# Kernel optimization log

Hardware: AMD Instinct MI355X
Metric: run time of the kernel (lower is better)

## Reference

```python
import jax, jax.numpy as jnp
import numpy as np

E = 1024       # embedding_dim
HQ = 16        # num_q_heads
G = 4          # group_size
HK = HQ // G   # num_kv_heads = 4
D = E // HQ    # q_head_dim = 64
B, N = 2, 2048


def setup_inputs() -> dict:
    key = jax.random.key(0)
    kx, kq, kk, kv, ko = jax.random.split(key, 5)
    scale = 0.02
    return {
        "x": jax.random.normal(kx, (B, N, E), dtype=jnp.float32),
        # weights stored as (in, out); torch Linear computes x @ W.T, equivalent math
        "Wq": jax.random.normal(kq, (E, E), dtype=jnp.float32) * scale,
        "Wk": jax.random.normal(kk, (E, E // G), dtype=jnp.float32) * scale,
        "Wv": jax.random.normal(kv, (E, E // G), dtype=jnp.float32) * scale,
        "Wo": jax.random.normal(ko, (E, E), dtype=jnp.float32) * scale,
    }


def reference(x, Wq, Wk, Wv, Wo):
    b, n, _ = x.shape
    q = x @ Wq                      # (b, n, E)
    k = x @ Wk                      # (b, n, HK*D)
    v = x @ Wv                      # (b, n, HK*D)
    # 'b n (h d) -> b h n d' then 'b (h g) n d -> b g h n d'  (h outer, g inner)
    q = q.reshape(b, n, HQ, D).transpose(0, 2, 1, 3)          # (b, HQ, n, D)
    q = q.reshape(b, HK, G, n, D).transpose(0, 2, 1, 3, 4)    # (b, G, HK, n, D)
    k = k.reshape(b, n, HK, D).transpose(0, 2, 1, 3)          # (b, HK, n, D)
    v = v.reshape(b, n, HK, D).transpose(0, 2, 1, 3)          # (b, HK, n, D)

    scores = jnp.einsum('bghnd,bhsd->bghns', q, k) / jnp.sqrt(jnp.float32(D))
    causal = jnp.triu(jnp.ones((n, n), dtype=bool), k=1)      # True above diagonal
    scores = jnp.where(causal[None, None, None], -jnp.inf, scores)
    probs = jax.nn.softmax(scores, axis=-1)                   # dropout p=0 -> no-op
    out = jnp.einsum('bghns,bhsd->bghnd', probs, v)           # (b, G, HK, n, D)
    # 'b g h n d -> b n (h g) d -> b n (h g d)'
    out = out.transpose(0, 3, 2, 1, 4).reshape(b, n, E)
    return out @ Wo
```

## Files before the change

kernel.cpp:

```cpp
#include <hip/hip_runtime.h>
#include <hip/hip_bf16.h>
#include <math.h>

#define Bsz 2
#define Nseq 2048
#define Edim 1024
#define HQ 16
#define HK 4
#define Dh 64
#define ROWS (Bsz * Nseq)
#define QKVW 1536
#define SCL 0.1803368801111244f

typedef __attribute__((ext_vector_type(8))) short short8;
typedef __attribute__((ext_vector_type(4))) float f32x4;

union S8U { short8 s8; unsigned u[4]; };

__device__ __forceinline__ ushort f2bf_u(float f) {
    union { __hip_bfloat16 h; ushort u; } c;
    c.h = __float2bfloat16(f);
    return c.u;
}
__device__ __forceinline__ unsigned bfpk(float lo, float hi) {
    return ((unsigned)f2bf_u(hi) << 16) | (unsigned)f2bf_u(lo);
}

__device__ __forceinline__ void gld16(const void* g, void* l) {
    __builtin_amdgcn_global_load_lds(
        (const __attribute__((address_space(1))) unsigned*)g,
        (__attribute__((address_space(3))) unsigned*)l, 16, 0, 0);
}

__global__ __launch_bounds__(256) void castx(const float* __restrict__ x,
                                             ushort* __restrict__ xb) {
    size_t i = ((size_t)blockIdx.x * 256 + threadIdx.x) * 8;
    float4 a = *(const float4*)(x + i);
    float4 c = *(const float4*)(x + i + 4);
    short8 v;
    v[0] = f2bf_u(a.x); v[1] = f2bf_u(a.y); v[2] = f2bf_u(a.z); v[3] = f2bf_u(a.w);
    v[4] = f2bf_u(c.x); v[5] = f2bf_u(c.y); v[6] = f2bf_u(c.z); v[7] = f2bf_u(c.w);
    *(short8*)(xb + i) = v;
}

__global__ __launch_bounds__(256) void tcastAll(const float* __restrict__ Wq,
                                                const float* __restrict__ Wk,
                                                const float* __restrict__ Wv,
                                                const float* __restrict__ Wo,
                                                ushort* __restrict__ WqkvT,
                                                ushort* __restrict__ WoT) {
    __shared__ float tle[32][33];
    int bid = blockIdx.x;
    const float* src; ushort* dst; int N; float sc = 1.0f;
    if (bid < 1024)      { src = Wq; dst = WqkvT;                          N = 1024; sc = SCL; }
    else if (bid < 1280) { src = Wk; dst = WqkvT + (size_t)1024 * 1024;    N = 256;  bid -= 1024; }
    else if (bid < 1536) { src = Wv; dst = WqkvT + (size_t)1280 * 1024;    N = 256;  bid -= 1280; }
    else                 { src = Wo; dst = WoT;                            N = 1024; bid -= 1536; }
    int nj = N >> 5;
    int j0 = (bid % nj) * 32, k0 = (bid / nj) * 32;
    int tx = threadIdx.x & 31, ty = threadIdx.x >> 5;
#pragma unroll
    for (int i = ty; i < 32; i += 8)
        tle[i][tx] = src[(size_t)(k0 + i) * N + j0 + tx];
    __syncthreads();
#pragma unroll
    for (int i = ty; i < 32; i += 8)
        dst[(size_t)(j0 + i) * 1024 + k0 + tx] = f2bf_u(tle[tx][i] * sc);
}

template<int WRITE_BF16>
__global__ __launch_bounds__(256) void gemm_bt(const ushort* __restrict__ A,
                                               const ushort* __restrict__ BT,
                                               void* __restrict__ Cout,
                                               int M, int N, int K) {
    __shared__ __attribute__((aligned(16))) ushort As[2][4][128][8];
    __shared__ __attribute__((aligned(16))) ushort Bs[2][4][64][8];
    const int tid = threadIdx.x;
    const int l = tid & 63, li = l & 15, lg = l >> 4;
    const int w = tid >> 6;
    const int wr = w >> 1, wc = w & 1;
    const int row0 = blockIdx.y * 128, col0 = blockIdx.x * 64;

    f32x4 acc[4][2];
#pragma unroll
    for (int i = 0; i < 4; ++i)
#pragma unroll
        for (int j = 0; j < 2; ++j) {
            acc[i][j][0] = 0.f; acc[i][j][1] = 0.f;
            acc[i][j][2] = 0.f; acc[i][j][3] = 0.f;
        }

    const int nk = K >> 5;

#define G_STAGE(buf, kk)                                                        \
    {                                                                           \
        int k0 = (kk) << 5;                                                     \
        _Pragma("unroll")                                                       \
        for (int i = 0; i < 3; ++i) {                                           \
            int id = w + i * 4;                                                 \
            if (id < 8) {                                                       \
                int g = id >> 1, h = id & 1;                                    \
                gld16(A + (size_t)(row0 + h * 64 + l) * K + k0 + g * 8,         \
                      &As[buf][g][h * 64][0]);                                  \
            } else {                                                            \
                int g = id - 8;                                                 \
                gld16(BT + (size_t)(col0 + l) * K + k0 + g * 8,                 \
                      &Bs[buf][g][0][0]);                                       \
            }                                                                   \
        }                                                                       \
    }

    G_STAGE(0, 0);
    __syncthreads();
    int buf = 0;
    for (int kk = 0; kk < nk; ++kk) {
        if (kk + 1 < nk) G_STAGE(buf ^ 1, kk + 1);
        short8 af[4], bfr[2];
#pragma unroll
        for (int mt = 0; mt < 4; ++mt)
            af[mt] = *(const short8*)&As[buf][lg][wr * 64 + mt * 16 + li][0];
#pragma unroll
        for (int nt = 0; nt < 2; ++nt)
            bfr[nt] = *(const short8*)&Bs[buf][lg][wc * 32 + nt * 16 + li][0];
#pragma unroll
        for (int mt = 0; mt < 4; ++mt)
#pragma unroll
            for (int nt = 0; nt < 2; ++nt)
                acc[mt][nt] = __builtin_amdgcn_mfma_f32_16x16x32_bf16(
                    af[mt], bfr[nt], acc[mt][nt], 0, 0, 0);
        __syncthreads();
        buf ^= 1;
    }
#undef G_STAGE

    if (WRITE_BF16) {
        ushort* C = (ushort*)Cout;
#pragma unroll
        for (int mt = 0; mt < 4; ++mt)
#pragma unroll
            for (int r = 0; r < 4; ++r) {
                int rg = row0 + wr * 64 + mt * 16 + lg * 4 + r;
#pragma unroll
                for (int nt = 0; nt < 2; ++nt)
                    C[(size_t)rg * N + col0 + wc * 32 + nt * 16 + li] =
                        f2bf_u(acc[mt][nt][r]);
            }
    } else {
        float* C = (float*)Cout;
#pragma unroll
        for (int mt = 0; mt < 4; ++mt)
#pragma unroll
            for (int r = 0; r < 4; ++r) {
                int rg = row0 + wr * 64 + mt * 16 + lg * 4 + r;
#pragma unroll
                for (int nt = 0; nt < 2; ++nt)
                    C[(size_t)rg * N + col0 + wc * 32 + nt * 16 + li] =
                        acc[mt][nt][r];
            }
    }
}

__global__ __launch_bounds__(256) void attn_mfma(const ushort* __restrict__ qkv,
                                                 ushort* __restrict__ o) {
    __shared__ __attribute__((aligned(16))) char smem[40960];
    ushort (*Ks)[8][64][8] = (ushort (*)[8][64][8])smem;
    unsigned (*VtD)[2048]  = (unsigned (*)[2048])(smem + 16384);
    ushort (*Ps)[8][16][8] = (ushort (*)[8][16][8])(smem + 32768);

    const int tid = threadIdx.x;
    const int l = tid & 63, li = l & 15, lg = l >> 4;
    const int w = tid >> 6;
    const int bx = blockIdx.x;
    const int hq = blockIdx.y, b = blockIdx.z, hk = hq >> 2;

    const int kp = 2 * (tid & 31), d0v = (tid >> 5) * 8;
    const int gv = kp >> 3, prv = (kp & 7) >> 1;

    const ushort* base  = qkv + (size_t)b * Nseq * QKVW;
    const ushort* vbase = base + 1280 + hk * 64 + d0v;
    const int qloc = w * 16 + li;

    for (int hseg = 0; hseg < 2; ++hseg) {
        const int qt = hseg ? (31 - bx) : bx;
        const int r0 = qt * 64;

        short8 q8[2];
#pragma unroll
        for (int c = 0; c < 2; ++c)
            q8[c] = *(const short8*)(base + (size_t)(r0 + qloc) * QKVW +
                                     hq * 64 + (c * 4 + lg) * 8);

#pragma unroll
        for (int i = 0; i < 2; ++i) {
            int g = w + i * 4;
            gld16(base + (size_t)l * QKVW + 1024 + hk * 64 + g * 8,
                  &Ks[0][g][0][0]);
        }
        short8 va = *(const short8*)(vbase + (size_t)kp * QKVW);
        short8 vb = *(const short8*)(vbase + (size_t)(kp + 1) * QKVW);
        __syncthreads();
        {
            S8U ua, ub; ua.s8 = va; ub.s8 = vb;
#pragma unroll
            for (int j = 0; j < 4; ++j) {
                VtD[0][gv * 256 + (((d0v + 2 * j) * 4 + prv) ^ (gv << 2))] =
                    __builtin_amdgcn_perm(ub.u[j], ua.u[j], 0x05040100u);
                VtD[0][gv * 256 + (((d0v + 2 * j + 1) * 4 + prv) ^ (gv << 2))] =
                    __builtin_amdgcn_perm(ub.u[j], ua.u[j], 0x07060302u);
            }
        }
        __syncthreads();

        f32x4 oacc[4];
#pragma unroll
        for (int dt = 0; dt < 4; ++dt) {
            oacc[dt][0] = 0.f; oacc[dt][1] = 0.f;
            oacc[dt][2] = 0.f; oacc[dt][3] = 0.f;
        }
        float m = -INFINITY, lsum = 0.f;

        for (int t = 0; t <= qt; ++t) {
            const int cur = t & 1, nxt = cur ^ 1;
            const bool pre = (t < qt);
            short8 vna, vnb;
            if (pre) {
                const int s1 = (t + 1) * 64;
#pragma unroll
                for (int i = 0; i < 2; ++i) {
                    int g = w + i * 4;
                    gld16(base + (size_t)(s1 + l) * QKVW + 1024 + hk * 64 + g * 8,
                          &Ks[nxt][g][0][0]);
                }
                const ushort* vr = vbase + (size_t)(s1 + kp) * QKVW;
                vna = *(const short8*)vr;
                vnb = *(const short8*)(vr + QKVW);
            }

            f32x4 s[4];
#pragma unroll
            for (int kb = 0; kb < 4; ++kb) {
                s[kb][0] = 0.f; s[kb][1] = 0.f; s[kb][2] = 0.f; s[kb][3] = 0.f;
            }
#pragma unroll
            for (int c = 0; c < 2; ++c)
#pragma unroll
                for (int kb = 0; kb < 4; ++kb) {
                    short8 bk = *(const short8*)&Ks[cur][c * 4 + lg][kb * 16 + li][0];
                    s[kb] = __builtin_amdgcn_mfma_f32_16x16x32_bf16(bk, q8[c], s[kb], 0, 0, 0);
                }

            float p[16];
            const bool last = (t == qt);
#pragma unroll
            for (int kb = 0; kb < 4; ++kb)
#pragma unroll
                for (int r = 0; r < 4; ++r) {
                    float sv = s[kb][r];
                    if (last && (kb * 16 + lg * 4 + r > qloc)) sv = -INFINITY;
                    p[kb * 4 + r] = sv;
                }

            float mx = fmaxf(fmaxf(
                fmaxf(fmaxf(p[0], p[1]), fmaxf(p[2], p[3])),
                fmaxf(fmaxf(p[4], p[5]), fmaxf(p[6], p[7]))),
                fmaxf(fmaxf(fmaxf(p[8], p[9]), fmaxf(p[10], p[11])),
                      fmaxf(fmaxf(p[12], p[13]), fmaxf(p[14], p[15]))));
            mx = fmaxf(mx, __shfl_xor(mx, 16, 64));
            mx = fmaxf(mx, __shfl_xor(mx, 32, 64));

            if (__any(mx - m > 8.0f)) {
                float mn = fmaxf(m, mx);
                float al = exp2f(m - mn);
                m = mn;
                lsum *= al;
                float alr[4];
#pragma unroll
                for (int r = 0; r < 4; ++r) alr[r] = __shfl(al, lg * 4 + r, 64);
#pragma unroll
                for (int dt = 0; dt < 4; ++dt)
#pragma unroll
                    for (int r = 0; r < 4; ++r) oacc[dt][r] *= alr[r];
            }

            float sum = 0.f;
#pragma unroll
            for (int i = 0; i < 16; ++i) {
                float e = exp2f(p[i] - m);
                p[i] = e;
                sum += e;
            }
            sum += __shfl_xor(sum, 16, 64);
            sum += __shfl_xor(sum, 32, 64);
            lsum += sum;

#pragma unroll
            for (int kb = 0; kb < 4; ++kb) {
                unsigned lo = bfpk(p[kb * 4 + 0], p[kb * 4 + 1]);
                unsigned hi = bfpk(p[kb * 4 + 2], p[kb * 4 + 3]);
                *(unsigned long long*)&Ps[w][2 * kb + (lg >> 1)][li][(lg & 1) * 4] =
                    ((unsigned long long)hi << 32) | (unsigned long long)lo;
            }

            if (pre) {
                S8U ua, ub; ua.s8 = vna; ub.s8 = vnb;
#pragma unroll
                for (int j = 0; j < 4; ++j) {
                    VtD[nxt][gv * 256 + (((d0v + 2 * j) * 4 + prv) ^ (gv << 2))] =
                        __builtin_amdgcn_perm(ub.u[j], ua.u[j], 0x05040100u);
                    VtD[nxt][gv * 256 + (((d0v + 2 * j + 1) * 4 + prv) ^ (gv << 2))] =
                        __builtin_amdgcn_perm(ub.u[j], ua.u[j], 0x07060302u);
                }
            }

#pragma unroll
            for (int c = 0; c < 2; ++c) {
                short8 pa = *(const short8*)&Ps[w][c * 4 + lg][li][0];
#pragma unroll
                for (int dt = 0; dt < 4; ++dt) {
                    int g = c * 4 + lg, d = dt * 16 + li;
                    short8 bv = *(const short8*)(&VtD[cur][g * 256 + ((d * 4) ^ (g << 2))]);
                    oacc[dt] = __builtin_amdgcn_mfma_f32_16x16x32_bf16(pa, bv, oacc[dt], 0, 0, 0);
                }
            }
            __syncthreads();
        }

        float linv[4];
#pragma unroll
        for (int r = 0; r < 4; ++r) linv[r] = 1.0f / __shfl(lsum, lg * 4 + r, 64);
#pragma unroll
        for (int r = 0; r < 4; ++r) {
            int rg = b * Nseq + r0 + w * 16 + lg * 4 + r;
#pragma unroll
            for (int dt = 0; dt < 4; ++dt)
                o[(size_t)rg * Edim + hq * 64 + dt * 16 + li] =
                    f2bf_u(oacc[dt][r] * linv[r]);
        }
    }
}

extern "C" void kernel_launch(void* const* d_in, const int* in_sizes, int n_in,
                              void* d_out, int out_size, void* d_ws, size_t ws_size,
                              hipStream_t stream) {
    const float* x  = (const float*)d_in[0];
    const float* Wq = (const float*)d_in[1];
    const float* Wk = (const float*)d_in[2];
    const float* Wv = (const float*)d_in[3];
    const float* Wo = (const float*)d_in[4];

    ushort* ws    = (ushort*)d_ws;
    ushort* xb    = ws;
    ushort* WqkvT = xb + (size_t)ROWS * Edim;
    ushort* WoT   = WqkvT + (size_t)QKVW * Edim;
    ushort* qkv   = WoT + (size_t)Edim * Edim;
    ushort* at    = qkv + (size_t)ROWS * QKVW;

    castx<<<ROWS * Edim / (256 * 8), 256, 0, stream>>>(x, xb);
    tcastAll<<<2560, 256, 0, stream>>>(Wq, Wk, Wv, Wo, WqkvT, WoT);

    gemm_bt<1><<<dim3(QKVW / 64, ROWS / 128), 256, 0, stream>>>(
        xb, WqkvT, qkv, ROWS, QKVW, Edim);

    attn_mfma<<<dim3(Nseq / 128, HQ, Bsz), 256, 0, stream>>>(qkv, at);

    gemm_bt<0><<<dim3(Edim / 64, ROWS / 128), 256, 0, stream>>>(
        at, WoT, d_out, ROWS, Edim, Edim);
}
```

Before: 209.3 us.

## Merge prep kernels, deepen GEMM K-tile, process KV tiles in pairs in attention

Fuses the x cast and weight transpose-cast into one prep launch, saving a kernel launch. The GEMM now stages 64-wide K slices instead of 32, halving the barrier count per block. The attention kernel loads two 64-key tiles per iteration and does one online-softmax rescale per 128 keys, cutting syncs and rescale work. In exchange, shared memory grows to 72KB in attention, which may lower occupancy, and odd tile counts waste one fully masked 64-key tile.

```diff
diff --git a/kernel.cpp b/kernel.cpp
--- a/kernel.cpp
+++ b/kernel.cpp
@@ -32,25 +32,26 @@
         (__attribute__((address_space(3))) unsigned*)l, 16, 0, 0);
 }
 
-__global__ __launch_bounds__(256) void castx(const float* __restrict__ x,
-                                             ushort* __restrict__ xb) {
-    size_t i = ((size_t)blockIdx.x * 256 + threadIdx.x) * 8;
-    float4 a = *(const float4*)(x + i);
-    float4 c = *(const float4*)(x + i + 4);
-    short8 v;
-    v[0] = f2bf_u(a.x); v[1] = f2bf_u(a.y); v[2] = f2bf_u(a.z); v[3] = f2bf_u(a.w);
-    v[4] = f2bf_u(c.x); v[5] = f2bf_u(c.y); v[6] = f2bf_u(c.z); v[7] = f2bf_u(c.w);
-    *(short8*)(xb + i) = v;
-}
-
-__global__ __launch_bounds__(256) void tcastAll(const float* __restrict__ Wq,
-                                                const float* __restrict__ Wk,
-                                                const float* __restrict__ Wv,
-                                                const float* __restrict__ Wo,
-                                                ushort* __restrict__ WqkvT,
-                                                ushort* __restrict__ WoT) {
+__global__ __launch_bounds__(256) void prep(const float* __restrict__ x,
+                                            const float* __restrict__ Wq,
+                                            const float* __restrict__ Wk,
+                                            const float* __restrict__ Wv,
+                                            const float* __restrict__ Wo,
+                                            ushort* __restrict__ xb,
+                                            ushort* __restrict__ WqkvT,
+                                            ushort* __restrict__ WoT) {
+    if (blockIdx.x < 2048) {
+        size_t i = ((size_t)blockIdx.x * 256 + threadIdx.x) * 8;
+        float4 a = *(const float4*)(x + i);
+        float4 c = *(const float4*)(x + i + 4);
+        short8 v;
+        v[0] = f2bf_u(a.x); v[1] = f2bf_u(a.y); v[2] = f2bf_u(a.z); v[3] = f2bf_u(a.w);
+        v[4] = f2bf_u(c.x); v[5] = f2bf_u(c.y); v[6] = f2bf_u(c.z); v[7] = f2bf_u(c.w);
+        *(short8*)(xb + i) = v;
+        return;
+    }
     __shared__ float tle[32][33];
-    int bid = blockIdx.x;
+    int bid = blockIdx.x - 2048;
     const float* src; ushort* dst; int N; float sc = 1.0f;
     if (bid < 1024)      { src = Wq; dst = WqkvT;                          N = 1024; sc = SCL; }
     else if (bid < 1280) { src = Wk; dst = WqkvT + (size_t)1024 * 1024;    N = 256;  bid -= 1024; }
@@ -73,8 +74,8 @@
                                                const ushort* __restrict__ BT,
                                                void* __restrict__ Cout,
                                                int M, int N, int K) {
-    __shared__ __attribute__((aligned(16))) ushort As[2][4][128][8];
-    __shared__ __attribute__((aligned(16))) ushort Bs[2][4][64][8];
+    __shared__ __attribute__((aligned(16))) ushort As[2][8][128][8];
+    __shared__ __attribute__((aligned(16))) ushort Bs[2][8][64][8];
     const int tid = threadIdx.x;
     const int l = tid & 63, li = l & 15, lg = l >> 4;
     const int w = tid >> 6;
@@ -90,20 +91,20 @@
             acc[i][j][2] = 0.f; acc[i][j][3] = 0.f;
         }
 
-    const int nk = K >> 5;
+    const int nk = K >> 6;
 
 #define G_STAGE(buf, kk)                                                        \
     {                                                                           \
-        int k0 = (kk) << 5;                                                     \
+        int k0 = (kk) << 6;                                                     \
         _Pragma("unroll")                                                       \
-        for (int i = 0; i < 3; ++i) {                                           \
+        for (int i = 0; i < 6; ++i) {                                           \
             int id = w + i * 4;                                                 \
-            if (id < 8) {                                                       \
+            if (id < 16) {                                                      \
                 int g = id >> 1, h = id & 1;                                    \
                 gld16(A + (size_t)(row0 + h * 64 + l) * K + k0 + g * 8,         \
                       &As[buf][g][h * 64][0]);                                  \
             } else {                                                            \
-                int g = id - 8;                                                 \
+                int g = id - 16;                                                \
                 gld16(BT + (size_t)(col0 + l) * K + k0 + g * 8,                 \
                       &Bs[buf][g][0][0]);                                       \
             }                                                                   \
@@ -115,19 +116,22 @@
     int buf = 0;
     for (int kk = 0; kk < nk; ++kk) {
         if (kk + 1 < nk) G_STAGE(buf ^ 1, kk + 1);
-        short8 af[4], bfr[2];
-#pragma unroll
-        for (int mt = 0; mt < 4; ++mt)
-            af[mt] = *(const short8*)&As[buf][lg][wr * 64 + mt * 16 + li][0];
-#pragma unroll
-        for (int nt = 0; nt < 2; ++nt)
-            bfr[nt] = *(const short8*)&Bs[buf][lg][wc * 32 + nt * 16 + li][0];
-#pragma unroll
-        for (int mt = 0; mt < 4; ++mt)
+#pragma unroll
+        for (int ks = 0; ks < 2; ++ks) {
+            short8 af[4], bfr[2];
+#pragma unroll
+            for (int mt = 0; mt < 4; ++mt)
+                af[mt] = *(const short8*)&As[buf][ks * 4 + lg][wr * 64 + mt * 16 + li][0];
 #pragma unroll
             for (int nt = 0; nt < 2; ++nt)
-                acc[mt][nt] = __builtin_amdgcn_mfma_f32_16x16x32_bf16(
-                    af[mt], bfr[nt], acc[mt][nt], 0, 0, 0);
+                bfr[nt] = *(const short8*)&Bs[buf][ks * 4 + lg][wc * 32 + nt * 16 + li][0];
+#pragma unroll
+            for (int mt = 0; mt < 4; ++mt)
+#pragma unroll
+                for (int nt = 0; nt < 2; ++nt)
+                    acc[mt][nt] = __builtin_amdgcn_mfma_f32_16x16x32_bf16(
+                        af[mt], bfr[nt], acc[mt][nt], 0, 0, 0);
+        }
         __syncthreads();
         buf ^= 1;
     }
@@ -162,10 +166,10 @@
 
 __global__ __launch_bounds__(256) void attn_mfma(const ushort* __restrict__ qkv,
                                                  ushort* __restrict__ o) {
-    __shared__ __attribute__((aligned(16))) char smem[40960];
-    ushort (*Ks)[8][64][8] = (ushort (*)[8][64][8])smem;
-    unsigned (*VtD)[2048]  = (unsigned (*)[2048])(smem + 16384);
-    ushort (*Ps)[8][16][8] = (ushort (*)[8][16][8])(smem + 32768);
+    __shared__ __attribute__((aligned(16))) char smem[73728];
+    ushort (*Ks)[2][8][64][8] = (ushort (*)[2][8][64][8])smem;
+    unsigned (*VtD)[2][2048]  = (unsigned (*)[2][2048])(smem + 32768);
+    ushort (*Ps)[8][16][8]    = (ushort (*)[8][16][8])(smem + 65536);
 
     const int tid = threadIdx.x;
     const int l = tid & 63, li = l & 15, lg = l >> 4;
@@ -183,6 +187,7 @@
     for (int hseg = 0; hseg < 2; ++hseg) {
         const int qt = hseg ? (31 - bx) : bx;
         const int r0 = qt * 64;
+        const int npair = (qt + 2) >> 1;
 
         short8 q8[2];
 #pragma unroll
@@ -191,22 +196,29 @@
                                      hq * 64 + (c * 4 + lg) * 8);
 
 #pragma unroll
-        for (int i = 0; i < 2; ++i) {
-            int g = w + i * 4;
-            gld16(base + (size_t)l * QKVW + 1024 + hk * 64 + g * 8,
-                  &Ks[0][g][0][0]);
-        }
-        short8 va = *(const short8*)(vbase + (size_t)kp * QKVW);
-        short8 vb = *(const short8*)(vbase + (size_t)(kp + 1) * QKVW);
+        for (int i = 0; i < 4; ++i) {
+            int id = w + i * 4, tile = id >> 3, g = id & 7;
+            gld16(base + (size_t)(tile * 64 + l) * QKVW + 1024 + hk * 64 + g * 8,
+                  &Ks[0][tile][g][0][0]);
+        }
+        short8 v0a = *(const short8*)(vbase + (size_t)kp * QKVW);
+        short8 v0b = *(const short8*)(vbase + (size_t)(kp + 1) * QKVW);
+        short8 v1a = *(const short8*)(vbase + (size_t)(64 + kp) * QKVW);
+        short8 v1b = *(const short8*)(vbase + (size_t)(64 + kp + 1) * QKVW);
         __syncthreads();
         {
-            S8U ua, ub; ua.s8 = va; ub.s8 = vb;
+            S8U ua0, ub0, ua1, ub1;
+            ua0.s8 = v0a; ub0.s8 = v0b; ua1.s8 = v1a; ub1.s8 = v1b;
 #pragma unroll
             for (int j = 0; j < 4; ++j) {
-                VtD[0][gv * 256 + (((d0v + 2 * j) * 4 + prv) ^ (gv << 2))] =
-                    __builtin_amdgcn_perm(ub.u[j], ua.u[j], 0x05040100u);
-                VtD[0][gv * 256 + (((d0v + 2 * j + 1) * 4 + prv) ^ (gv << 2))] =
-                    __builtin_amdgcn_perm(ub.u[j], ua.u[j], 0x07060302u);
+                VtD[0][0][gv * 256 + (((d0v + 2 * j) * 4 + prv) ^ (gv << 2))] =
+                    __builtin_amdgcn_perm(ub0.u[j], ua0.u[j], 0x05040100u);
+                VtD[0][0][gv * 256 + (((d0v + 2 * j + 1) * 4 + prv) ^ (gv << 2))] =
+                    __builtin_amdgcn_perm(ub0.u[j], ua0.u[j], 0x07060302u);
+                VtD[0][1][gv * 256 + (((d0v + 2 * j) * 4 + prv) ^ (gv << 2))] =
+                    __builtin_amdgcn_perm(ub1.u[j], ua1.u[j], 0x05040100u);
+                VtD[0][1][gv * 256 + (((d0v + 2 * j + 1) * 4 + prv) ^ (gv << 2))] =
+                    __builtin_amdgcn_perm(ub1.u[j], ua1.u[j], 0x07060302u);
             }
         }
         __syncthreads();
@@ -219,52 +231,55 @@
         }
         float m = -INFINITY, lsum = 0.f;
 
-        for (int t = 0; t <= qt; ++t) {
-            const int cur = t & 1, nxt = cur ^ 1;
-            const bool pre = (t < qt);
-            short8 vna, vnb;
+        for (int pt = 0; pt < npair; ++pt) {
+            const int cur = pt & 1, nxt = cur ^ 1;
+            const bool pre = (pt + 1 < npair);
+            short8 vn0a, vn0b, vn1a, vn1b;
             if (pre) {
-                const int s1 = (t + 1) * 64;
-#pragma unroll
-                for (int i = 0; i < 2; ++i) {
-                    int g = w + i * 4;
-                    gld16(base + (size_t)(s1 + l) * QKVW + 1024 + hk * 64 + g * 8,
-                          &Ks[nxt][g][0][0]);
-                }
-                const ushort* vr = vbase + (size_t)(s1 + kp) * QKVW;
-                vna = *(const short8*)vr;
-                vnb = *(const short8*)(vr + QKVW);
-            }
-
-            f32x4 s[4];
-#pragma unroll
-            for (int kb = 0; kb < 4; ++kb) {
-                s[kb][0] = 0.f; s[kb][1] = 0.f; s[kb][2] = 0.f; s[kb][3] = 0.f;
-            }
-#pragma unroll
-            for (int c = 0; c < 2; ++c)
+                const int s1 = (pt + 1) * 128;
+#pragma unroll
+                for (int i = 0; i < 4; ++i) {
+                    int id = w + i * 4, tile = id >> 3, g = id & 7;
+                    gld16(base + (size_t)(s1 + tile * 64 + l) * QKVW + 1024 + hk * 64 + g * 8,
+                          &Ks[nxt][tile][g][0][0]);
+                }
+                vn0a = *(const short8*)(vbase + (size_t)(s1 + kp) * QKVW);
+                vn0b = *(const short8*)(vbase + (size_t)(s1 + kp + 1) * QKVW);
+                vn1a = *(const short8*)(vbase + (size_t)(s1 + 64 + kp) * QKVW);
+                vn1b = *(const short8*)(vbase + (size_t)(s1 + 64 + kp + 1) * QKVW);
+            }
+
+            float p[32];
+#pragma unroll
+            for (int tt = 0; tt < 2; ++tt) {
+                f32x4 s[4];
 #pragma unroll
                 for (int kb = 0; kb < 4; ++kb) {
-                    short8 bk = *(const short8*)&Ks[cur][c * 4 + lg][kb * 16 + li][0];
-                    s[kb] = __builtin_amdgcn_mfma_f32_16x16x32_bf16(bk, q8[c], s[kb], 0, 0, 0);
-                }
-
-            float p[16];
-            const bool last = (t == qt);
-#pragma unroll
-            for (int kb = 0; kb < 4; ++kb)
-#pragma unroll
-                for (int r = 0; r < 4; ++r) {
-                    float sv = s[kb][r];
-                    if (last && (kb * 16 + lg * 4 + r > qloc)) sv = -INFINITY;
-                    p[kb * 4 + r] = sv;
-                }
-
-            float mx = fmaxf(fmaxf(
-                fmaxf(fmaxf(p[0], p[1]), fmaxf(p[2], p[3])),
-                fmaxf(fmaxf(p[4], p[5]), fmaxf(p[6], p[7]))),
-                fmaxf(fmaxf(fmaxf(p[8], p[9]), fmaxf(p[10], p[11])),
-                      fmaxf(fmaxf(p[12], p[13]), fmaxf(p[14], p[15]))));
+                    s[kb][0] = 0.f; s[kb][1] = 0.f; s[kb][2] = 0.f; s[kb][3] = 0.f;
+                }
+#pragma unroll
+                for (int c = 0; c < 2; ++c)
+#pragma unroll
+                    for (int kb = 0; kb < 4; ++kb) {
+                        short8 bk = *(const short8*)&Ks[cur][tt][c * 4 + lg][kb * 16 + li][0];
+                        s[kb] = __builtin_amdgcn_mfma_f32_16x16x32_bf16(bk, q8[c], s[kb], 0, 0, 0);
+                    }
+                const int tglob = pt * 2 + tt;
+                const bool diag = (tglob == qt), over = (tglob > qt);
+#pragma unroll
+                for (int kb = 0; kb < 4; ++kb)
+#pragma unroll
+                    for (int r = 0; r < 4; ++r) {
+                        float sv = s[kb][r];
+                        if (over || (diag && (kb * 16 + lg * 4 + r > qloc)))
+                            sv = -INFINITY;
+                        p[tt * 16 + kb * 4 + r] = sv;
+                    }
+            }
+
+            float mx = p[0];
+#pragma unroll
+            for (int i = 1; i < 32; ++i) mx = fmaxf(mx, p[i]);
             mx = fmaxf(mx, __shfl_xor(mx, 16, 64));
             mx = fmaxf(mx, __shfl_xor(mx, 32, 64));
 
@@ -284,7 +299,7 @@
 
             float sum = 0.f;
 #pragma unroll
-            for (int i = 0; i < 16; ++i) {
+            for (int i = 0; i < 32; ++i) {
                 float e = exp2f(p[i] - m);
                 p[i] = e;
                 sum += e;
@@ -293,33 +308,40 @@
             sum += __shfl_xor(sum, 32, 64);
             lsum += sum;
 
-#pragma unroll
-            for (int kb = 0; kb < 4; ++kb) {
-                unsigned lo = bfpk(p[kb * 4 + 0], p[kb * 4 + 1]);
-                unsigned hi = bfpk(p[kb * 4 + 2], p[kb * 4 + 3]);
-                *(unsigned long long*)&Ps[w][2 * kb + (lg >> 1)][li][(lg & 1) * 4] =
-                    ((unsigned long long)hi << 32) | (unsigned long long)lo;
-            }
-
             if (pre) {
-                S8U ua, ub; ua.s8 = vna; ub.s8 = vnb;
+                S8U ua0, ub0, ua1, ub1;
+                ua0.s8 = vn0a; ub0.s8 = vn0b; ua1.s8 = vn1a; ub1.s8 = vn1b;
 #pragma unroll
                 for (int j = 0; j < 4; ++j) {
-                    VtD[nxt][gv * 256 + (((d0v + 2 * j) * 4 + prv) ^ (gv << 2))] =
-                        __builtin_amdgcn_perm(ub.u[j], ua.u[j], 0x05040100u);
-                    VtD[nxt][gv * 256 + (((d0v + 2 * j + 1) * 4 + prv) ^ (gv << 2))] =
-                        __builtin_amdgcn_perm(ub.u[j], ua.u[j], 0x07060302u);
-                }
-            }
-
-#pragma unroll
-            for (int c = 0; c < 2; ++c) {
-                short8 pa = *(const short8*)&Ps[w][c * 4 + lg][li][0];
-#pragma unroll
-                for (int dt = 0; dt < 4; ++dt) {
-                    int g = c * 4 + lg, d = dt * 16 + li;
-                    short8 bv = *(const short8*)(&VtD[cur][g * 256 + ((d * 4) ^ (g << 2))]);
-                    oacc[dt] = __builtin_amdgcn_mfma_f32_16x16x32_bf16(pa, bv, oacc[dt], 0, 0, 0);
+                    VtD[nxt][0][gv * 256 + (((d0v + 2 * j) * 4 + prv) ^ (gv << 2))] =
+                        __builtin_amdgcn_perm(ub0.u[j], ua0.u[j], 0x05040100u);
+                    VtD[nxt][0][gv * 256 + (((d0v + 2 * j + 1) * 4 + prv) ^ (gv << 2))] =
+                        __builtin_amdgcn_perm(ub0.u[j], ua0.u[j], 0x07060302u);
+                    VtD[nxt][1][gv * 256 + (((d0v + 2 * j) * 4 + prv) ^ (gv << 2))] =
+                        __builtin_amdgcn_perm(ub1.u[j], ua1.u[j], 0x05040100u);
+                    VtD[nxt][1][gv * 256 + (((d0v + 2 * j + 1) * 4 + prv) ^ (gv << 2))] =
+                        __builtin_amdgcn_perm(ub1.u[j], ua1.u[j], 0x07060302u);
+                }
+            }
+
+#pragma unroll
+            for (int tt = 0; tt < 2; ++tt) {
+#pragma unroll
+                for (int kb = 0; kb < 4; ++kb) {
+                    unsigned lo = bfpk(p[tt * 16 + kb * 4 + 0], p[tt * 16 + kb * 4 + 1]);
+                    unsigned hi = bfpk(p[tt * 16 + kb * 4 + 2], p[tt * 16 + kb * 4 + 3]);
+                    *(unsigned long long*)&Ps[w][2 * kb + (lg >> 1)][li][(lg & 1) * 4] =
+                        ((unsigned long long)hi << 32) | (unsigned long long)lo;
+                }
+#pragma unroll
+                for (int c = 0; c < 2; ++c) {
+                    short8 pa = *(const short8*)&Ps[w][c * 4 + lg][li][0];
+#pragma unroll
+                    for (int dt = 0; dt < 4; ++dt) {
+                        int g = c * 4 + lg, d = dt * 16 + li;
+                        short8 bv = *(const short8*)(&VtD[cur][tt][g * 256 + ((d * 4) ^ (g << 2))]);
+                        oacc[dt] = __builtin_amdgcn_mfma_f32_16x16x32_bf16(pa, bv, oacc[dt], 0, 0, 0);
+                    }
                 }
             }
             __syncthreads();
@@ -355,8 +377,7 @@
     ushort* qkv   = WoT + (size_t)Edim * Edim;
     ushort* at    = qkv + (size_t)ROWS * QKVW;
 
-    castx<<<ROWS * Edim / (256 * 8), 256, 0, stream>>>(x, xb);
-    tcastAll<<<2560, 256, 0, stream>>>(Wq, Wk, Wv, Wo, WqkvT, WoT);
+    prep<<<4608, 256, 0, stream>>>(x, Wq, Wk, Wv, Wo, xb, WqkvT, WoT);
 
     gemm_bt<1><<<dim3(QKVW / 64, ROWS / 128), 256, 0, stream>>>(
         xb, WqkvT, qkv, ROWS, QKVW, Edim);
```

Measured after the change: 215.8 us. +3.1%, slower.

## Widen GEMM tiles to 128x128, swizzle block order, merge prep kernels

Applied to the files above, without the earlier changes.

The two cast kernels are merged into one prep launch, removing a launch. The GEMM tile grows from 128x64 to 128x128, so each wave computes a 64x64 subtile with 16 MFMA accumulators, giving more reuse per LDS load. Blocks are launched on a 1D grid and remapped with a stride-8 swizzle, likely to spread neighbouring blocks across XCDs. The cost is half as many blocks (384 for QKV, 256 for the output projection), which may underfill the CUs, plus higher register pressure.

```diff
diff --git a/kernel.cpp b/kernel.cpp
--- a/kernel.cpp
+++ b/kernel.cpp
@@ -32,25 +32,26 @@
         (__attribute__((address_space(3))) unsigned*)l, 16, 0, 0);
 }
 
-__global__ __launch_bounds__(256) void castx(const float* __restrict__ x,
-                                             ushort* __restrict__ xb) {
-    size_t i = ((size_t)blockIdx.x * 256 + threadIdx.x) * 8;
-    float4 a = *(const float4*)(x + i);
-    float4 c = *(const float4*)(x + i + 4);
-    short8 v;
-    v[0] = f2bf_u(a.x); v[1] = f2bf_u(a.y); v[2] = f2bf_u(a.z); v[3] = f2bf_u(a.w);
-    v[4] = f2bf_u(c.x); v[5] = f2bf_u(c.y); v[6] = f2bf_u(c.z); v[7] = f2bf_u(c.w);
-    *(short8*)(xb + i) = v;
-}
-
-__global__ __launch_bounds__(256) void tcastAll(const float* __restrict__ Wq,
-                                                const float* __restrict__ Wk,
-                                                const float* __restrict__ Wv,
-                                                const float* __restrict__ Wo,
-                                                ushort* __restrict__ WqkvT,
-                                                ushort* __restrict__ WoT) {
+__global__ __launch_bounds__(256) void prep(const float* __restrict__ x,
+                                            const float* __restrict__ Wq,
+                                            const float* __restrict__ Wk,
+                                            const float* __restrict__ Wv,
+                                            const float* __restrict__ Wo,
+                                            ushort* __restrict__ xb,
+                                            ushort* __restrict__ WqkvT,
+                                            ushort* __restrict__ WoT) {
+    if (blockIdx.x < 2048) {
+        size_t i = ((size_t)blockIdx.x * 256 + threadIdx.x) * 8;
+        float4 a = *(const float4*)(x + i);
+        float4 c = *(const float4*)(x + i + 4);
+        short8 v;
+        v[0] = f2bf_u(a.x); v[1] = f2bf_u(a.y); v[2] = f2bf_u(a.z); v[3] = f2bf_u(a.w);
+        v[4] = f2bf_u(c.x); v[5] = f2bf_u(c.y); v[6] = f2bf_u(c.z); v[7] = f2bf_u(c.w);
+        *(short8*)(xb + i) = v;
+        return;
+    }
     __shared__ float tle[32][33];
-    int bid = blockIdx.x;
+    int bid = blockIdx.x - 2048;
     const float* src; ushort* dst; int N; float sc = 1.0f;
     if (bid < 1024)      { src = Wq; dst = WqkvT;                          N = 1024; sc = SCL; }
     else if (bid < 1280) { src = Wk; dst = WqkvT + (size_t)1024 * 1024;    N = 256;  bid -= 1024; }
@@ -72,20 +73,24 @@
 __global__ __launch_bounds__(256) void gemm_bt(const ushort* __restrict__ A,
                                                const ushort* __restrict__ BT,
                                                void* __restrict__ Cout,
-                                               int M, int N, int K) {
+                                               int N, int K, int nx) {
     __shared__ __attribute__((aligned(16))) ushort As[2][4][128][8];
-    __shared__ __attribute__((aligned(16))) ushort Bs[2][4][64][8];
+    __shared__ __attribute__((aligned(16))) ushort Bs[2][4][128][8];
     const int tid = threadIdx.x;
     const int l = tid & 63, li = l & 15, lg = l >> 4;
     const int w = tid >> 6;
     const int wr = w >> 1, wc = w & 1;
-    const int row0 = blockIdx.y * 128, col0 = blockIdx.x * 64;
-
-    f32x4 acc[4][2];
+
+    const int lin = blockIdx.x;
+    const int q = gridDim.x >> 3;
+    const int swz = (lin & 7) * q + (lin >> 3);
+    const int row0 = (swz / nx) * 128, col0 = (swz % nx) * 128;
+
+    f32x4 acc[4][4];
 #pragma unroll
     for (int i = 0; i < 4; ++i)
 #pragma unroll
-        for (int j = 0; j < 2; ++j) {
+        for (int j = 0; j < 4; ++j) {
             acc[i][j][0] = 0.f; acc[i][j][1] = 0.f;
             acc[i][j][2] = 0.f; acc[i][j][3] = 0.f;
         }
@@ -96,17 +101,13 @@
     {                                                                           \
         int k0 = (kk) << 5;                                                     \
         _Pragma("unroll")                                                       \
-        for (int i = 0; i < 3; ++i) {                                           \
+        for (int i = 0; i < 2; ++i) {                                           \
             int id = w + i * 4;                                                 \
-            if (id < 8) {                                                       \
-                int g = id >> 1, h = id & 1;                                    \
-                gld16(A + (size_t)(row0 + h * 64 + l) * K + k0 + g * 8,         \
-                      &As[buf][g][h * 64][0]);                                  \
-            } else {                                                            \
-                int g = id - 8;                                                 \
-                gld16(BT + (size_t)(col0 + l) * K + k0 + g * 8,                 \
-                      &Bs[buf][g][0][0]);                                       \
-            }                                                                   \
+            int g = id >> 1, h = id & 1;                                        \
+            gld16(A + (size_t)(row0 + h * 64 + l) * K + k0 + g * 8,             \
+                  &As[buf][g][h * 64][0]);                                      \
+            gld16(BT + (size_t)(col0 + h * 64 + l) * K + k0 + g * 8,            \
+                  &Bs[buf][g][h * 64][0]);                                      \
         }                                                                       \
     }
 
@@ -115,17 +116,17 @@
     int buf = 0;
     for (int kk = 0; kk < nk; ++kk) {
         if (kk + 1 < nk) G_STAGE(buf ^ 1, kk + 1);
-        short8 af[4], bfr[2];
+        short8 af[4], bfr[4];
 #pragma unroll
         for (int mt = 0; mt < 4; ++mt)
             af[mt] = *(const short8*)&As[buf][lg][wr * 64 + mt * 16 + li][0];
 #pragma unroll
-        for (int nt = 0; nt < 2; ++nt)
-            bfr[nt] = *(const short8*)&Bs[buf][lg][wc * 32 + nt * 16 + li][0];
+        for (int nt = 0; nt < 4; ++nt)
+            bfr[nt] = *(const short8*)&Bs[buf][lg][wc * 64 + nt * 16 + li][0];
 #pragma unroll
         for (int mt = 0; mt < 4; ++mt)
 #pragma unroll
-            for (int nt = 0; nt < 2; ++nt)
+            for (int nt = 0; nt < 4; ++nt)
                 acc[mt][nt] = __builtin_amdgcn_mfma_f32_16x16x32_bf16(
                     af[mt], bfr[nt], acc[mt][nt], 0, 0, 0);
         __syncthreads();
@@ -141,8 +142,8 @@
             for (int r = 0; r < 4; ++r) {
                 int rg = row0 + wr * 64 + mt * 16 + lg * 4 + r;
 #pragma unroll
-                for (int nt = 0; nt < 2; ++nt)
-                    C[(size_t)rg * N + col0 + wc * 32 + nt * 16 + li] =
+                for (int nt = 0; nt < 4; ++nt)
+                    C[(size_t)rg * N + col0 + wc * 64 + nt * 16 + li] =
                         f2bf_u(acc[mt][nt][r]);
             }
     } else {
@@ -153,8 +154,8 @@
             for (int r = 0; r < 4; ++r) {
                 int rg = row0 + wr * 64 + mt * 16 + lg * 4 + r;
 #pragma unroll
-                for (int nt = 0; nt < 2; ++nt)
-                    C[(size_t)rg * N + col0 + wc * 32 + nt * 16 + li] =
+                for (int nt = 0; nt < 4; ++nt)
+                    C[(size_t)rg * N + col0 + wc * 64 + nt * 16 + li] =
                         acc[mt][nt][r];
             }
     }
@@ -355,14 +356,13 @@
     ushort* qkv   = WoT + (size_t)Edim * Edim;
     ushort* at    = qkv + (size_t)ROWS * QKVW;
 
-    castx<<<ROWS * Edim / (256 * 8), 256, 0, stream>>>(x, xb);
-    tcastAll<<<2560, 256, 0, stream>>>(Wq, Wk, Wv, Wo, WqkvT, WoT);
-
-    gemm_bt<1><<<dim3(QKVW / 64, ROWS / 128), 256, 0, stream>>>(
-        xb, WqkvT, qkv, ROWS, QKVW, Edim);
+    prep<<<4608, 256, 0, stream>>>(x, Wq, Wk, Wv, Wo, xb, WqkvT, WoT);
+
+    gemm_bt<1><<<(QKVW / 128) * (ROWS / 128), 256, 0, stream>>>(
+        xb, WqkvT, qkv, QKVW, Edim, QKVW / 128);
 
     attn_mfma<<<dim3(Nseq / 128, HQ, Bsz), 256, 0, stream>>>(qkv, at);
 
-    gemm_bt<0><<<dim3(Edim / 64, ROWS / 128), 256, 0, stream>>>(
-        at, WoT, d_out, ROWS, Edim, Edim);
-}
+    gemm_bt<0><<<(Edim / 128) * (ROWS / 128), 256, 0, stream>>>(
+        at, WoT, d_out, Edim, Edim, Edim / 128);
+}
```

New measurement: 206.4 us. Within noise of the previous version (-1.4%).
